# Performance work log

Measured on AMD Instinct MI355X. Metric: run time of the kernel, lower is better.

The kernel has to match this reference:

```python
import jax, jax.numpy as jnp
import numpy as np

V = 78864; E = 300; H = 512; A = 300; T = 20; DEC_EMB = 512; START = 2


def _pos_encoding(n, d):
    pos = np.arange(n)[:, None].astype(np.float32)
    i = np.arange(d)[None, :]
    angle = pos / np.power(10000.0, (2 * (i // 2)).astype(np.float32) / d)
    pe = np.where(i % 2 == 0, np.sin(angle), np.cos(angle)).astype(np.float32)
    return jnp.asarray(pe)  # [n, d]


def _lstm_cell(x, h, c, Wih, Whh, b):
    g = x @ Wih.T + h @ Whh.T + b
    i, f, gg, o = jnp.split(g, 4, axis=-1)
    c = jax.nn.sigmoid(f) * c + jax.nn.sigmoid(i) * jnp.tanh(gg)
    h = jax.nn.sigmoid(o) * jnp.tanh(c)
    return h, c


def setup_inputs() -> dict:
    key = jax.random.key(0)
    ks = iter(jax.random.split(key, 48))
    B, L = 40, 1000
    def w(shape, s=0.02):
        return jax.random.normal(next(ks), shape, jnp.float32) * s
    def z(shape):
        return jnp.zeros(shape, jnp.float32)
    inp = dict(
        enc_in=jax.random.randint(next(ks), (B, L), 0, V),
        enc_out=jax.random.normal(next(ks), (B, L, H), jnp.float32),
        enc_mask=jnp.zeros((B, L), bool),
        inputs=jax.random.randint(next(ks), (B, T), 0, V),
        embed=w((V, E)),
        elmo1_Wih=w((4 * H, E)), elmo1_Whh=w((4 * H, H)), elmo1_b=z((4 * H,)),
        elmo2_Wih=w((4 * H, H)), elmo2_Whh=w((4 * H, H)), elmo2_b=z((4 * H,)),
        in_W=w((DEC_EMB, H + E + A + H)), in_b=z((DEC_EMB,)),
        rnn1_Wih=w((4 * H, DEC_EMB)), rnn1_Whh=w((4 * H, H)), rnn1_b=z((4 * H,)),
        att1_Wq=w((A, H)), att1_bq=z((A,)), att1_Wk=w((A, H)), att1_bk=z((A,)), att1_Wv=w((A, H)), att1_bv=z((A,)),
        rnn2_Wih=w((4 * H, A)), rnn2_Whh=w((4 * H, H)), rnn2_b=z((4 * H,)),
        att2_Wq=w((A, H)), att2_bq=z((A,)), att2_Wk=w((A, H)), att2_bk=z((A,)), att2_Wv=w((A, H)), att2_bv=z((A,)),
        copy_W=w((A, H)), copy_b=z((A,)),
        out_W=w((V, A)), out_b=z((V,)),
        scale=jnp.asarray(1.0, jnp.float32),
    )
    return inp


def _forward(enc_in, enc_out, enc_mask, inputs, embed,
             elmo1_Wih, elmo1_Whh, elmo1_b, elmo2_Wih, elmo2_Whh, elmo2_b,
             in_W, in_b, rnn1_Wih, rnn1_Whh, rnn1_b,
             att1_Wq, att1_bq, att1_Wk, att1_bk, att1_Wv, att1_bv,
             rnn2_Wih, rnn2_Whh, rnn2_b,
             att2_Wq, att2_bq, att2_Wk, att2_bk, att2_Wv, att2_bv,
             copy_W, copy_b, out_W, out_b, scale):
    B, L = enc_in.shape
    pe = _pos_encoding(T, DEC_EMB)  # [T, 512]
    # Precompute per-encoder projections (hoisted out of the step loop).
    K1 = jnp.einsum('blh,ah->bla', enc_out, att1_Wk) + att1_bk
    V1 = jnp.einsum('blh,ah->bla', enc_out, att1_Wv) + att1_bv
    K2 = jnp.einsum('blh,ah->bla', enc_out, att2_Wk) + att2_bk
    V2 = jnp.einsum('blh,ah->bla', enc_out, att2_Wv) + att2_bv
    copyK = jnp.tanh(jnp.einsum('blh,ah->bla', enc_out, copy_W) + copy_b)
    bidx = jnp.arange(B)[:, None]

    def attn(h, Wq, bq, K, Vp):
        q = h @ Wq.T + bq                          # [B, A]
        s = jnp.einsum('ba,bla->bl', q, K)
        s = jnp.where(enc_mask, -1e9, s)
        p = jax.nn.softmax(s, axis=-1)
        return jnp.einsum('bl,bla->ba', p, Vp)

    # teacher forcing with random_int=0 -> always use ground-truth inputs
    sym_in = jnp.concatenate([jnp.full((B, 1), START, inputs.dtype), inputs[:, :-1]], axis=1).T  # [T,B]
    sym_out = inputs.T  # [T,B]

    zf = lambda *s: jnp.zeros(s, enc_out.dtype)
    carry0 = (zf(B, H), zf(B, H), zf(B, H), zf(B, H),  # elmo h1,c1,h2,c2
              zf(B, H), zf(B, H), zf(B, H), zf(B, H),  # rnn1 h,c ; rnn2 h,c
              zf(B, A), zf(B, H))                       # dec_att_out, select_read

    def step(carry, xs):
        eh1, ec1, eh2, ec2, h1, c1, h2, c2, att, sel = carry
        pe_t, s_in, s_out = xs
        emb = embed[s_in]                                           # [B, E]
        eh1, ec1 = _lstm_cell(emb, eh1, ec1, elmo1_Wih, elmo1_Whh, elmo1_b)
        eh2, ec2 = _lstm_cell(eh1, eh2, ec2, elmo2_Wih, elmo2_Whh, elmo2_b)
        in_embed = jnp.concatenate([emb, eh2], axis=-1)              # [B, 812]
        dec_in = jnp.concatenate([in_embed, att, sel], axis=-1) @ in_W.T + in_b + pe_t
        h1, c1 = _lstm_cell(dec_in, h1, c1, rnn1_Wih, rnn1_Whh, rnn1_b)
        att = attn(h1, att1_Wq, att1_bq, K1, V1)
        h2, c2 = _lstm_cell(att, h2, c2, rnn2_Wih, rnn2_Whh, rnn2_b)
        att = attn(h2, att2_Wq, att2_bq, K2, V2) + att
        # copy scores
        s = jnp.einsum('ba,bla->bl', att, copyK)
        s = jnp.where(enc_mask, -1e9, s)
        score_c = jax.nn.softmax(s, axis=-1)
        score_e = score_c * scale * scale
        vocab = att @ out_W.T + out_b                                # [B, V]
        vocab = vocab.at[bidx, enc_in].add(score_e)
        sym_pred = jnp.argmax(vocab, axis=-1).astype(jnp.int32)
        eq = (enc_in == s_out[:, None]).astype(score_c.dtype)
        score_f = score_c * eq
        score_f = score_f / (jnp.sum(score_f, axis=-1, keepdims=True) + 1e-8)
        sel = jnp.einsum('bl,blh->bh', score_f, enc_out)
        return (eh1, ec1, eh2, ec2, h1, c1, h2, c2, att, sel), (vocab, sym_pred)

    _, (dec_out, syms) = jax.lax.scan(step, carry0, (pe, sym_in, sym_out))
    return jnp.transpose(dec_out, (1, 0, 2)), syms.T  # [B,T,V], [B,T]


def reference(enc_in, enc_out, enc_mask, inputs, embed,
              elmo1_Wih, elmo1_Whh, elmo1_b, elmo2_Wih, elmo2_Whh, elmo2_b,
              in_W, in_b, rnn1_Wih, rnn1_Whh, rnn1_b,
              att1_Wq, att1_bq, att1_Wk, att1_bk, att1_Wv, att1_bv,
              rnn2_Wih, rnn2_Whh, rnn2_b,
              att2_Wq, att2_bq, att2_Wk, att2_bk, att2_Wv, att2_bv,
              copy_W, copy_b, out_W, out_b, scale):
    return _forward(enc_in, enc_out, enc_mask, inputs, embed,
                    elmo1_Wih, elmo1_Whh, elmo1_b, elmo2_Wih, elmo2_Whh, elmo2_b,
                    in_W, in_b, rnn1_Wih, rnn1_Whh, rnn1_b,
                    att1_Wq, att1_bq, att1_Wk, att1_bk, att1_Wv, att1_bv,
                    rnn2_Wih, rnn2_Whh, rnn2_b,
                    att2_Wq, att2_bq, att2_Wk, att2_bk, att2_Wv, att2_bv,
                    copy_W, copy_b, out_W, out_b, scale)
```

## Files before the change

### kernel.cpp

```cpp
#include <hip/hip_runtime.h>
#include <math.h>

#define B_ 40
#define L_ 1000
#define H_ 512
#define A_ 300
#define T_ 20
#define E_ 300
#define V_ 78864
#define START_ 2

#define NBLK 256
#define NTHR 512

#define OFF_COPYK 0ul
#define OFF_M1T   12000000ul
#define OFF_M2T   12262144ul
#define OFF_BQK1  12524288ul
#define OFF_BQK2  12524800ul
#define OFF_QK    12525312ul
#define OFF_DEC   12545792ul
#define OFF_ATT1  12566272ul
#define OFF_ATTT  12578272ul
#define OFF_CPART 12590272ul
#define OFF_CSTAT 12713152ul
#define OFF_SCC   12713664ul
#define OFF_STT   12753664ul
#define OFF_ATT2  13081344ul
#define OFF_SELP  13093344ul
#define OFF_CNT   13216224ul
#define WS_END    13216288ul

struct P {
  const int* enc_in; const float* enc; const unsigned char* mask; const int* inputs;
  const float* embed;
  const float *e1Wih,*e1Whh,*e1b,*e2Wih,*e2Whh,*e2b;
  const float *inW,*inb;
  const float *r1Wih,*r1Whh,*r1b;
  const float *a1Wq,*a1bq,*a1Wk,*a1Wv,*a1bv;
  const float *r2Wih,*r2Whh,*r2b;
  const float *a2Wq,*a2bq,*a2Wk,*a2Wv,*a2bv;
  const float *cW,*cb,*oW,*ob,*scale;
  float* dout;
  float *copyK,*M1T,*M2T,*bqk1,*bqk2,*qk,*dec,*att1,*attT,*cpart,*cstat,*scc,*stt,*att2,*selp;
  unsigned* cnt;
};

__device__ __forceinline__ float sigm(float x){ return 1.0f/(1.0f+expf(-x)); }

__device__ __forceinline__ float wredSum(float v){
#pragma unroll
  for(int o=32;o>0;o>>=1) v+=__shfl_xor(v,o);
  return v;
}
__device__ __forceinline__ float wredMax(float v){
#pragma unroll
  for(int o=32;o>0;o>>=1) v=fmaxf(v,__shfl_xor(v,o));
  return v;
}

__device__ __forceinline__ void gbar(unsigned* cnt, unsigned target){
  __syncthreads();
  if(threadIdx.x==0){
    __hip_atomic_fetch_add(cnt,1u,__ATOMIC_RELEASE,__HIP_MEMORY_SCOPE_AGENT);
    while(__hip_atomic_load(cnt,__ATOMIC_RELAXED,__HIP_MEMORY_SCOPE_AGENT)<target){
      __builtin_amdgcn_s_sleep(1);
    }
    (void)__hip_atomic_load(cnt,__ATOMIC_ACQUIRE,__HIP_MEMORY_SCOPE_AGENT);
  }
  __syncthreads();
}

template<typename SRC>
static __device__ __forceinline__ void gv_accum(float* xs,int K,const float* Wrow,
    float& acc,int lane,int kq,int nq,SRC src){
  for(int k0=0;k0<K;k0+=256){
    int ch=min(256,K-k0);
    __syncthreads();
    for(int i=threadIdx.x;i<40*ch;i+=NTHR){
      int bb=i/ch, kk=i-bb*ch;
      xs[bb*257+kk]=src(bb,k0+kk);
    }
    __syncthreads();
    if(lane<40){
#pragma unroll 4
      for(int k=kq;k<ch;k+=nq) acc+=Wrow[k0+k]*xs[lane*257+k];
    }
  }
}

static __device__ void lstm_ph(const P& p,float* SH,float* gld,int t,
    const float* Wih,int XD,const float* Whh,const float* bias,
    const float* xvec,bool gather,
    const float* hr,const float* cr,float* hw,float* cw){
  int tid=threadIdx.x,w=tid>>6,lane=tid&63;
  int gate=w&3,usub=w>>2;
  int row=gate*H_+(blockIdx.x*2+usub);
  int rowu=__builtin_amdgcn_readfirstlane(row);
  float acc=bias[rowu];
  const float* W1=Wih+(size_t)rowu*XD;
  if(gather){
    const int* inp=p.inputs; const float* emb=p.embed; int tt=t;
    gv_accum(SH,XD,W1,acc,lane,0,1,[=](int bb,int kk)->float{
      int si=(tt==0)?START_:inp[bb*T_+tt-1];
      return emb[(size_t)si*E_+kk];});
  }else{
    gv_accum(SH,XD,W1,acc,lane,0,1,[=](int bb,int kk)->float{
      return xvec[(size_t)bb*XD+kk];});
  }
  const float* W2=Whh+(size_t)rowu*H_;
  gv_accum(SH,H_,W2,acc,lane,0,1,[=](int bb,int kk)->float{
    return hr[bb*H_+kk];});
  gld[w*64+lane]=acc;
  __syncthreads();
  if(w<2&&lane<40){
    int u=blockIdx.x*2+w,b=lane;
    float gi=gld[(w*4+0)*64+b],gf=gld[(w*4+1)*64+b],gg=gld[(w*4+2)*64+b],go=gld[(w*4+3)*64+b];
    float c=cr[b*H_+u];
    float cn=sigm(gf)*c+sigm(gi)*tanhf(gg);
    hw[b*H_+u]=sigm(go)*tanhf(cn);
    cw[b*H_+u]=cn;
  }
  __syncthreads();
}

static __device__ void qk_ph(const P& p,float* SH,const float* hsrc,
    const float* MT,const float* bqk){
  int tid=threadIdx.x;
  if(blockIdx.x>=240) return;
  int b=blockIdx.x/6, j=blockIdx.x%6;
  SH[tid]=hsrc[b*H_+tid];
  __syncthreads();
  int h0=j*86, hc=min(86,H_-h0);
  if(tid<hc){
    int hp=h0+tid;
    float a=bqk[hp];
    const float4* mr=(const float4*)(MT+(size_t)hp*H_);
#pragma unroll 8
    for(int i=0;i<H_/4;i++){
      float4 m4=mr[i];
      a+=SH[4*i]*m4.x+SH[4*i+1]*m4.y+SH[4*i+2]*m4.z+SH[4*i+3]*m4.w;
    }
    p.qk[b*H_+hp]=a;
  }
}

static __device__ void scctx_ph(const P& p,float* SH,float* red){
  int tid=threadIdx.x,w=tid>>6,lane=tid&63;
  if(blockIdx.x>=240) return;
  int b=blockIdx.x/6, j=blockIdx.x%6;
  int l0=j*167, lcnt=min(167,L_-l0);
  const float* qrow=p.qk+b*H_;
  float4 q0=*(const float4*)(qrow+lane*8);
  float4 q1=*(const float4*)(qrow+lane*8+4);
  float m=-3.0e38f,S=0.f;
  float4 a0=make_float4(0.f,0.f,0.f,0.f), a1=a0;
  for(int l=l0+w;l<l0+lcnt;l+=8){
    const float4* er=(const float4*)(p.enc+((size_t)(b*L_+l))*H_);
    float4 e0=er[lane*2], e1=er[lane*2+1];
    float pp=q0.x*e0.x+q0.y*e0.y+q0.z*e0.z+q0.w*e0.w
            +q1.x*e1.x+q1.y*e1.y+q1.z*e1.z+q1.w*e1.w;
    pp=wredSum(pp);
    if(p.mask[b*L_+l]) pp=-1e9f;
    float mn=fmaxf(m,pp);
    float sc=expf(m-mn), pe=expf(pp-mn);
    S=S*sc+pe;
    a0.x=a0.x*sc+pe*e0.x; a0.y=a0.y*sc+pe*e0.y; a0.z=a0.z*sc+pe*e0.z; a0.w=a0.w*sc+pe*e0.w;
    a1.x=a1.x*sc+pe*e1.x; a1.y=a1.y*sc+pe*e1.y; a1.z=a1.z*sc+pe*e1.z; a1.w=a1.w*sc+pe*e1.w;
    m=mn;
  }
  *(float4*)(SH+w*H_+lane*8)=a0;
  *(float4*)(SH+w*H_+lane*8+4)=a1;
  if(lane==0){red[w]=m; red[8+w]=S;}
  __syncthreads();
  float mb=red[0];
#pragma unroll
  for(int q=1;q<8;q++) mb=fmaxf(mb,red[q]);
  float Sb=0.f;
#pragma unroll
  for(int q=0;q<8;q++) Sb+=red[8+q]*expf(red[q]-mb);
  float pv=0.f;
#pragma unroll
  for(int q=0;q<8;q++) pv+=expf(red[q]-mb)*SH[q*H_+tid];
  p.cpart[(size_t)(b*6+j)*H_+tid]=pv;
  if(tid==0){p.cstat[(b*6+j)*2]=mb; p.cstat[(b*6+j)*2+1]=Sb;}
}

static __device__ void atto_ph(const P& p,float* SH,const float* Wv,const float* bv,bool ADD){
  int tid=threadIdx.x;
  if(blockIdx.x>=40) return;
  int b=blockIdx.x;
  float mb=-3.0e38f;
#pragma unroll
  for(int j=0;j<6;j++) mb=fmaxf(mb,p.cstat[(b*6+j)*2]);
  float Sb=0.f;
#pragma unroll
  for(int j=0;j<6;j++) Sb+=p.cstat[(b*6+j)*2+1]*expf(p.cstat[(b*6+j)*2]-mb);
  float inv=1.0f/Sb;
  float cx=0.f;
#pragma unroll
  for(int j=0;j<6;j++) cx+=expf(p.cstat[(b*6+j)*2]-mb)*p.cpart[(size_t)(b*6+j)*H_+tid];
  SH[tid]=cx*inv;
  __syncthreads();
  if(tid<A_){
    float a=bv[tid];
    const float4* wr=(const float4*)(Wv+(size_t)tid*H_);
#pragma unroll 8
    for(int i=0;i<H_/4;i++){
      float4 w4=wr[i];
      a+=SH[4*i]*w4.x+SH[4*i+1]*w4.y+SH[4*i+2]*w4.z+SH[4*i+3]*w4.w;
    }
    if(ADD){ a+=p.att1[b*A_+tid]; p.att2[b*A_+tid]=a; p.attT[tid*B_+b]=a; }
    else p.att1[b*A_+tid]=a;
  }
}

static __device__ void copysc_ph(const P& p){
  int tid=threadIdx.x,w=tid>>6,lane=tid&63;
  if(blockIdx.x>=240) return;
  int b=blockIdx.x/6, j=blockIdx.x%6;
  int l0=j*167, lcnt=min(167,L_-l0);
  float4 r0=*(const float4*)(p.att2+b*A_+lane*4);
  float4 r1=make_float4(0.f,0.f,0.f,0.f);
  if(lane<11) r1=*(const float4*)(p.att2+b*A_+256+lane*4);
  for(int l=l0+w;l<l0+lcnt;l+=8){
    const float4* cr=(const float4*)(p.copyK+((size_t)(b*L_+l))*A_);
    float4 c0=cr[lane];
    float pp=r0.x*c0.x+r0.y*c0.y+r0.z*c0.z+r0.w*c0.w;
    if(lane<11){
      float4 c1=cr[64+lane];
      pp+=r1.x*c1.x+r1.y*c1.y+r1.z*c1.z+r1.w*c1.w;
    }
    pp=wredSum(pp);
    if(lane==0) p.scc[b*L_+l]=p.mask[b*L_+l]?-1e9f:pp;
  }
}

static __device__ void vocab_ph(const P& p,float* SH,int t){
  int tid=threadIdx.x;
  int v0=blockIdx.x*312;
  if(v0>=V_) return;
  int vcnt=min(312,V_-v0);
  float acc[40];
#pragma unroll
  for(int b=0;b<40;b++) acc[b]=0.f;
  for(int c=0;c<10;c++){
    int a0=c*32, aw=min(32,A_-a0);
    __syncthreads();
    for(int i=tid;i<vcnt*aw;i+=NTHR){
      int vr=i/aw, ac=i-vr*aw;
      SH[vr*33+ac]=p.oW[(size_t)(v0+vr)*A_+a0+ac];
    }
    __syncthreads();
    if(tid<vcnt){
      for(int ac=0;ac<aw;ac++){
        float wv=SH[tid*33+ac];
        const float* at=p.attT+(a0+ac)*B_;
#pragma unroll
        for(int bq=0;bq<10;bq++){
          float4 t4=*(const float4*)(at+bq*4);
          acc[bq*4+0]+=wv*t4.x; acc[bq*4+1]+=wv*t4.y;
          acc[bq*4+2]+=wv*t4.z; acc[bq*4+3]+=wv*t4.w;
        }
      }
    }
  }
  if(tid<vcnt){
    int v=v0+tid;
    float obv=p.ob[v];
#pragma unroll
    for(int b=0;b<40;b++) p.dout[((size_t)(b*T_+t))*V_+v]=acc[b]+obv;
  }
}

static __device__ void scatsel_ph(const P& p,float* SH,float* red,int t){
  int tid=threadIdx.x,w=tid>>6,lane=tid&63;
  if(blockIdx.x>=240) return;
  int b=blockIdx.x/6, j=blockIdx.x%6;
  int l0=j*167, lcnt=min(167,L_-l0);
  for(int i=tid;i<L_;i+=NTHR) SH[i]=p.scc[b*L_+i];
  __syncthreads();
  float lm=-3.0e38f;
  for(int i=tid;i<L_;i+=NTHR) lm=fmaxf(lm,SH[i]);
  lm=wredMax(lm);
  if(lane==0) red[w]=lm;
  __syncthreads();
  float m=red[0];
#pragma unroll
  for(int q=1;q<8;q++) m=fmaxf(m,red[q]);
  __syncthreads();
  int so=p.inputs[b*T_+t];
  float ls=0.f,lq=0.f;
  for(int i=tid;i<L_;i+=NTHR){
    float exv=expf(SH[i]-m);
    ls+=exv;
    if(p.enc_in[b*L_+i]==so) lq+=exv;
  }
  ls=wredSum(ls); lq=wredSum(lq);
  if(lane==0){red[w]=ls; red[8+w]=lq;}
  __syncthreads();
  float S=0.f,Q=0.f;
#pragma unroll
  for(int q=0;q<8;q++){S+=red[q];Q+=red[8+q];}
  if(tid<lcnt){
    int l=l0+tid;
    float exv=expf(SH[l]-m);
    SH[1024+tid]=(p.enc_in[b*L_+l]==so)?exv:0.f;
    float sc2=p.scale[0]*p.scale[0];
    atomicAdd(p.dout+((size_t)(b*T_+t))*V_+p.enc_in[b*L_+l], exv*sc2/S);
  }
  __syncthreads();
  float inv=1.0f/(Q+1e-8f*S);
  float a=0.f;
  for(int li=0;li<lcnt;li++)
    a+=SH[1024+li]*p.enc[((size_t)(b*L_+l0+li))*H_+tid];
  p.selp[(size_t)(b*6+j)*H_+tid]=a*inv;
}

static __device__ void argmax_ph(const P& p,float* SH,int t){
  int tid=threadIdx.x;
  if(blockIdx.x>=40) return;
  int b=blockIdx.x;
  const float* row=p.dout+((size_t)(b*T_+t))*V_;
  float best=-3.0e38f; int bi=0;
  for(int i4=tid;i4<V_/4;i4+=NTHR){
    float4 x=((const float4*)row)[i4];
    int base=i4*4;
    if(x.x>best){best=x.x;bi=base;}
    if(x.y>best){best=x.y;bi=base+1;}
    if(x.z>best){best=x.z;bi=base+2;}
    if(x.w>best){best=x.w;bi=base+3;}
  }
  int* isa=(int*)(SH+512);
  SH[tid]=best; isa[tid]=bi;
  __syncthreads();
  for(int off=256;off>0;off>>=1){
    if(tid<off){
      float ov=SH[tid+off]; int oi=isa[tid+off];
      if(ov>SH[tid]||(ov==SH[tid]&&oi<isa[tid])){SH[tid]=ov; isa[tid]=oi;}
    }
    __syncthreads();
  }
  if(tid==0) p.dout[(size_t)B_*T_*V_+b*T_+t]=(float)isa[0];
}

__global__ __launch_bounds__(NTHR,2) void k_persist(P p){
  __shared__ float SH[10320];
  __shared__ float gld[512];
  __shared__ float red[16];
  int blk=blockIdx.x, tid=threadIdx.x;
  unsigned bt=0;
#define BARR() do{bt++; gbar(p.cnt,bt*(unsigned)NBLK);}while(0)

  {
    int mm=blk>>7, r0=(blk&127)*4;
    const float* Wq = mm? p.a2Wq : p.a1Wq;
    const float* Wk = mm? p.a2Wk : p.a1Wk;
    float* MT = mm? p.M2T : p.M1T;
    float s0=0.f,s1=0.f,s2=0.f,s3=0.f;
    for(int a=0;a<A_;a++){
      float wq=Wq[a*H_+tid];
      s0+=wq*Wk[a*H_+r0+0];
      s1+=wq*Wk[a*H_+r0+1];
      s2+=wq*Wk[a*H_+r0+2];
      s3+=wq*Wk[a*H_+r0+3];
    }
    MT[(size_t)(r0+0)*H_+tid]=s0;
    MT[(size_t)(r0+1)*H_+tid]=s1;
    MT[(size_t)(r0+2)*H_+tid]=s2;
    MT[(size_t)(r0+3)*H_+tid]=s3;
    if((blk&127)==0){
      const float* bq = mm? p.a2bq : p.a1bq;
      float ab=0.f;
      for(int a=0;a<A_;a++) ab+=bq[a]*Wk[a*H_+tid];
      (mm? p.bqk2 : p.bqk1)[tid]=ab;
    }
  }
  for(int item=blk;item<B_*63;item+=NBLK){
    int b=item/63, lt=item-b*63;
    int l0=lt*16, lcnt=min(16,L_-l0);
    float acc[16];
    float bv=(tid<A_)?p.cb[tid]:0.f;
#pragma unroll
    for(int l=0;l<16;l++) acc[l]=bv;
    for(int k0=0;k0<H_;k0+=32){
      __syncthreads();
      for(int i=tid;i<A_*32;i+=NTHR){
        int a=i>>5,kc=i&31;
        SH[a*33+kc]=p.cW[(size_t)a*H_+k0+kc];
      }
      __syncthreads();
      if(tid<A_){
#pragma unroll
        for(int l=0;l<16;l++){
          if(l<lcnt){
            const float* es=p.enc+((size_t)(b*L_+l0+l))*H_+k0;
            float al=acc[l];
#pragma unroll
            for(int kc=0;kc<32;kc++) al+=SH[tid*33+kc]*es[kc];
            acc[l]=al;
          }
        }
      }
    }
    if(tid<A_){
#pragma unroll
      for(int l=0;l<16;l++)
        if(l<lcnt) p.copyK[((size_t)(b*L_+l0+l))*A_+tid]=tanhf(acc[l]);
    }
  }
  BARR();

  for(int t=0;t<T_;t++){
    int rp=t&1, wp=rp^1;
    float* stt=p.stt;
    auto SL=[&](int i,int par){ return stt+((size_t)(i*2+par))*(B_*H_); };
    float *eh1r=SL(0,rp),*eh1w=SL(0,wp),*ec1r=SL(1,rp),*ec1w=SL(1,wp);
    float *eh2r=SL(2,rp),*eh2w=SL(2,wp),*ec2r=SL(3,rp),*ec2w=SL(3,wp);
    float *h1r=SL(4,rp),*h1w=SL(4,wp),*c1r=SL(5,rp),*c1w=SL(5,wp);
    float *h2r=SL(6,rp),*h2w=SL(6,wp),*c2r=SL(7,rp),*c2w=SL(7,wp);

    lstm_ph(p,SH,gld,t,p.e1Wih,E_,p.e1Whh,p.e1b,nullptr,true ,eh1r,ec1r,eh1w,ec1w); BARR();
    lstm_ph(p,SH,gld,t,p.e2Wih,H_,p.e2Whh,p.e2b,eh1w  ,false,eh2r,ec2r,eh2w,ec2w); BARR();

    {
      int w=tid>>6,lane=tid&63;
      int usub=w>>2, kq=w&3;
      int unit=blk*2+usub;
      int rowu=__builtin_amdgcn_readfirstlane(unit);
      float acc=0.f;
      const float* Wr=p.inW+(size_t)rowu*1624;
      const int* inp=p.inputs; const float* emb=p.embed;
      const float* e2=eh2w; const float* a2c=p.att2; const float* sp=p.selp;
      int tt=t;
      gv_accum(SH,1624,Wr,acc,lane,kq,4,[=](int bb,int kk)->float{
        if(kk<E_){int si=(tt==0)?START_:inp[bb*T_+tt-1];return emb[(size_t)si*E_+kk];}
        else if(kk<E_+H_) return e2[bb*H_+kk-E_];
        else if(kk<E_+H_+A_) return a2c[bb*A_+kk-(E_+H_)];
        else{
          int hh=kk-(E_+H_+A_); float s=0.f;
#pragma unroll
          for(int jj=0;jj<6;jj++) s+=sp[(size_t)(bb*6+jj)*H_+hh];
          return s;
        }
      });
      gld[(usub*4+kq)*64+lane]=acc;
      __syncthreads();
      if(w<2&&lane<40){
        int u=blk*2+w;
        float s=gld[(w*4+0)*64+lane]+gld[(w*4+1)*64+lane]
               +gld[(w*4+2)*64+lane]+gld[(w*4+3)*64+lane];
        float ex=(float)(2*(u>>1))/512.0f;
        float ang=(float)t/powf(10000.0f,ex);
        s+=p.inb[u]+((u&1)?cosf(ang):sinf(ang));
        p.dec[lane*H_+u]=s;
      }
      __syncthreads();
    }
    BARR();

    lstm_ph(p,SH,gld,t,p.r1Wih,H_,p.r1Whh,p.r1b,p.dec ,false,h1r,c1r,h1w,c1w); BARR();
    qk_ph(p,SH,h1w,p.M1T,p.bqk1);                                              BARR();
    scctx_ph(p,SH,red);                                                        BARR();
    atto_ph(p,SH,p.a1Wv,p.a1bv,false);                                         BARR();
    lstm_ph(p,SH,gld,t,p.r2Wih,A_,p.r2Whh,p.r2b,p.att1,false,h2r,c2r,h2w,c2w); BARR();
    qk_ph(p,SH,h2w,p.M2T,p.bqk2);                                              BARR();
    scctx_ph(p,SH,red);                                                        BARR();
    atto_ph(p,SH,p.a2Wv,p.a2bv,true);                                          BARR();
    copysc_ph(p);                                                              BARR();
    vocab_ph(p,SH,t);                                                          BARR();
    scatsel_ph(p,SH,red,t);                                                    BARR();
    argmax_ph(p,SH,t);
  }
#undef BARR
}

extern "C" void kernel_launch(void* const* d_in, const int* in_sizes, int n_in,
                              void* d_out, int out_size, void* d_ws, size_t ws_size,
                              hipStream_t stream){
  P p;
  p.enc_in=(const int*)d_in[0];
  p.enc   =(const float*)d_in[1];
  p.mask  =(const unsigned char*)d_in[2];
  p.inputs=(const int*)d_in[3];
  p.embed =(const float*)d_in[4];
  p.e1Wih=(const float*)d_in[5];  p.e1Whh=(const float*)d_in[6];  p.e1b=(const float*)d_in[7];
  p.e2Wih=(const float*)d_in[8];  p.e2Whh=(const float*)d_in[9];  p.e2b=(const float*)d_in[10];
  p.inW  =(const float*)d_in[11]; p.inb  =(const float*)d_in[12];
  p.r1Wih=(const float*)d_in[13]; p.r1Whh=(const float*)d_in[14]; p.r1b=(const float*)d_in[15];
  p.a1Wq =(const float*)d_in[16]; p.a1bq =(const float*)d_in[17];
  p.a1Wk =(const float*)d_in[18];
  p.a1Wv =(const float*)d_in[20]; p.a1bv =(const float*)d_in[21];
  p.r2Wih=(const float*)d_in[22]; p.r2Whh=(const float*)d_in[23]; p.r2b=(const float*)d_in[24];
  p.a2Wq =(const float*)d_in[25]; p.a2bq =(const float*)d_in[26];
  p.a2Wk =(const float*)d_in[27];
  p.a2Wv =(const float*)d_in[29]; p.a2bv =(const float*)d_in[30];
  p.cW   =(const float*)d_in[31]; p.cb   =(const float*)d_in[32];
  p.oW   =(const float*)d_in[33]; p.ob   =(const float*)d_in[34];
  p.scale=(const float*)d_in[35];
  p.dout=(float*)d_out;

  float* w=(float*)d_ws;
  p.copyK=w+OFF_COPYK;
  p.M1T  =w+OFF_M1T;   p.M2T =w+OFF_M2T;
  p.bqk1 =w+OFF_BQK1;  p.bqk2=w+OFF_BQK2;
  p.qk   =w+OFF_QK;    p.dec =w+OFF_DEC;
  p.att1 =w+OFF_ATT1;  p.attT=w+OFF_ATTT;
  p.cpart=w+OFF_CPART; p.cstat=w+OFF_CSTAT;
  p.scc  =w+OFF_SCC;   p.stt =w+OFF_STT;
  p.att2 =w+OFF_ATT2;  p.selp=w+OFF_SELP;
  p.cnt  =(unsigned*)(w+OFF_CNT);

  hipMemsetAsync(w+OFF_STT,0,(WS_END-OFF_STT)*sizeof(float),stream);
  k_persist<<<NBLK,NTHR,0,stream>>>(p);
}
```

Before: 18.03 ms.

## Store copy keys as padded bf16 and restructure attention context via LDS tiles

```diff
diff --git a/kernel.cpp b/kernel.cpp
--- a/kernel.cpp
+++ b/kernel.cpp
@@ -13,23 +13,23 @@
 #define NBLK 256
 #define NTHR 512
 
-#define OFF_COPYK 0ul
-#define OFF_M1T   12000000ul
-#define OFF_M2T   12262144ul
-#define OFF_BQK1  12524288ul
-#define OFF_BQK2  12524800ul
-#define OFF_QK    12525312ul
-#define OFF_DEC   12545792ul
-#define OFF_ATT1  12566272ul
-#define OFF_ATTT  12578272ul
-#define OFF_CPART 12590272ul
-#define OFF_CSTAT 12713152ul
-#define OFF_SCC   12713664ul
-#define OFF_STT   12753664ul
-#define OFF_ATT2  13081344ul
-#define OFF_SELP  13093344ul
-#define OFF_CNT   13216224ul
-#define WS_END    13216288ul
+#define OFF_CKH   0ul
+#define OFF_M1T   6400000ul
+#define OFF_M2T   6662144ul
+#define OFF_BQK1  6924288ul
+#define OFF_BQK2  6924800ul
+#define OFF_QK    6925312ul
+#define OFF_DEC   6945792ul
+#define OFF_ATT1  6966272ul
+#define OFF_ATTT  6978272ul
+#define OFF_CPART 6990272ul
+#define OFF_CSTAT 7113152ul
+#define OFF_SCC   7113664ul
+#define OFF_STT   7153664ul
+#define OFF_ATT2  7481344ul
+#define OFF_SELP  7493344ul
+#define OFF_CNT   7616224ul
+#define WS_END    7616288ul
 
 struct P {
   const int* enc_in; const float* enc; const unsigned char* mask; const int* inputs;
@@ -42,7 +42,8 @@
   const float *a2Wq,*a2bq,*a2Wk,*a2Wv,*a2bv;
   const float *cW,*cb,*oW,*ob,*scale;
   float* dout;
-  float *copyK,*M1T,*M2T,*bqk1,*bqk2,*qk,*dec,*att1,*attT,*cpart,*cstat,*scc,*stt,*att2,*selp;
+  unsigned short* copyKh;
+  float *M1T,*M2T,*bqk1,*bqk2,*qk,*dec,*att1,*attT,*cpart,*cstat,*scc,*stt,*att2,*selp;
   unsigned* cnt;
 };
 
@@ -57,6 +58,11 @@
 #pragma unroll
   for(int o=32;o>0;o>>=1) v=fmaxf(v,__shfl_xor(v,o));
   return v;
+}
+__device__ __forceinline__ unsigned short f2bf(float f){
+  unsigned u=__float_as_uint(f);
+  u=(u+0x7fffu+((u>>16)&1u))>>16;
+  return (unsigned short)u;
 }
 
 __device__ __forceinline__ void gbar(unsigned* cnt, unsigned target){
@@ -145,7 +151,7 @@
   }
 }
 
-static __device__ void scctx_ph(const P& p,float* SH,float* red){
+static __device__ void scctx_ph(const P& p,float* SH){
   int tid=threadIdx.x,w=tid>>6,lane=tid&63;
   if(blockIdx.x>=240) return;
   int b=blockIdx.x/6, j=blockIdx.x%6;
@@ -153,37 +159,49 @@
   const float* qrow=p.qk+b*H_;
   float4 q0=*(const float4*)(qrow+lane*8);
   float4 q1=*(const float4*)(qrow+lane*8+4);
-  float m=-3.0e38f,S=0.f;
-  float4 a0=make_float4(0.f,0.f,0.f,0.f), a1=a0;
-  for(int l=l0+w;l<l0+lcnt;l+=8){
-    const float4* er=(const float4*)(p.enc+((size_t)(b*L_+l))*H_);
-    float4 e0=er[lane*2], e1=er[lane*2+1];
-    float pp=q0.x*e0.x+q0.y*e0.y+q0.z*e0.z+q0.w*e0.w
-            +q1.x*e1.x+q1.y*e1.y+q1.z*e1.z+q1.w*e1.w;
-    pp=wredSum(pp);
-    if(p.mask[b*L_+l]) pp=-1e9f;
-    float mn=fmaxf(m,pp);
-    float sc=expf(m-mn), pe=expf(pp-mn);
-    S=S*sc+pe;
-    a0.x=a0.x*sc+pe*e0.x; a0.y=a0.y*sc+pe*e0.y; a0.z=a0.z*sc+pe*e0.z; a0.w=a0.w*sc+pe*e0.w;
-    a1.x=a1.x*sc+pe*e1.x; a1.y=a1.y*sc+pe*e1.y; a1.z=a1.z*sc+pe*e1.z; a1.w=a1.w*sc+pe*e1.w;
+  float* tile=SH;
+  float* sc16=SH+8192;
+  float m=-3.0e38f,S=0.f,acc=0.f;
+  for(int t0=0;t0<lcnt;t0+=16){
+    int tc=min(16,lcnt-t0);
+    __syncthreads();
+    {
+      const float4* src=(const float4*)(p.enc+((size_t)(b*L_+l0+t0))*H_);
+      float4* dst=(float4*)tile;
+      for(int i=tid;i<tc*128;i+=NTHR) dst[i]=src[i];
+    }
+    __syncthreads();
+#pragma unroll
+    for(int r=0;r<2;r++){
+      int row=w*2+r;
+      float sc;
+      if(row<tc){
+        const float4* er=(const float4*)(tile+row*512);
+        float4 e0=er[lane*2], e1=er[lane*2+1];
+        float pp=q0.x*e0.x+q0.y*e0.y+q0.z*e0.z+q0.w*e0.w
+                +q1.x*e1.x+q1.y*e1.y+q1.z*e1.z+q1.w*e1.w;
+        pp=wredSum(pp);
+        sc=p.mask[b*L_+l0+t0+row]?-1e9f:pp;
+      } else sc=-1e30f;
+      if(lane==0) sc16[row]=sc;
+    }
+    __syncthreads();
+    float tm=-3.0e38f;
+    for(int r=0;r<tc;r++) tm=fmaxf(tm,sc16[r]);
+    float mn=fmaxf(m,tm);
+    float scl=expf(m-mn);
+    float Sadd=0.f, aadd=0.f;
+    for(int r=0;r<tc;r++){
+      float pe=expf(sc16[r]-mn);
+      Sadd+=pe;
+      aadd+=pe*tile[r*512+tid];
+    }
+    S=S*scl+Sadd;
+    acc=acc*scl+aadd;
     m=mn;
   }
-  *(float4*)(SH+w*H_+lane*8)=a0;
-  *(float4*)(SH+w*H_+lane*8+4)=a1;
-  if(lane==0){red[w]=m; red[8+w]=S;}
-  __syncthreads();
-  float mb=red[0];
-#pragma unroll
-  for(int q=1;q<8;q++) mb=fmaxf(mb,red[q]);
-  float Sb=0.f;
-#pragma unroll
-  for(int q=0;q<8;q++) Sb+=red[8+q]*expf(red[q]-mb);
-  float pv=0.f;
-#pragma unroll
-  for(int q=0;q<8;q++) pv+=expf(red[q]-mb)*SH[q*H_+tid];
-  p.cpart[(size_t)(b*6+j)*H_+tid]=pv;
-  if(tid==0){p.cstat[(b*6+j)*2]=mb; p.cstat[(b*6+j)*2+1]=Sb;}
+  p.cpart[(size_t)(b*6+j)*H_+tid]=acc;
+  if(tid==0){p.cstat[(b*6+j)*2]=m; p.cstat[(b*6+j)*2+1]=S;}
 }
 
 static __device__ void atto_ph(const P& p,float* SH,const float* Wv,const float* bv,bool ADD){
@@ -220,16 +238,21 @@
   if(blockIdx.x>=240) return;
   int b=blockIdx.x/6, j=blockIdx.x%6;
   int l0=j*167, lcnt=min(167,L_-l0);
-  float4 r0=*(const float4*)(p.att2+b*A_+lane*4);
-  float4 r1=make_float4(0.f,0.f,0.f,0.f);
-  if(lane<11) r1=*(const float4*)(p.att2+b*A_+256+lane*4);
+  float ar[8];
+#pragma unroll
+  for(int q=0;q<8;q++){
+    int a=lane*8+q;
+    ar[q]=(lane<40&&a<A_)? p.att2[b*A_+a] : 0.f;
+  }
   for(int l=l0+w;l<l0+lcnt;l+=8){
-    const float4* cr=(const float4*)(p.copyK+((size_t)(b*L_+l))*A_);
-    float4 c0=cr[lane];
-    float pp=r0.x*c0.x+r0.y*c0.y+r0.z*c0.z+r0.w*c0.w;
-    if(lane<11){
-      float4 c1=cr[64+lane];
-      pp+=r1.x*c1.x+r1.y*c1.y+r1.z*c1.z+r1.w*c1.w;
+    float pp=0.f;
+    if(lane<40){
+      const uint4* cr=(const uint4*)(p.copyKh+((size_t)(b*L_+l))*320);
+      uint4 kk=cr[lane];
+      pp =ar[0]*__uint_as_float(kk.x<<16)+ar[1]*__uint_as_float(kk.x&0xffff0000u);
+      pp+=ar[2]*__uint_as_float(kk.y<<16)+ar[3]*__uint_as_float(kk.y&0xffff0000u);
+      pp+=ar[4]*__uint_as_float(kk.z<<16)+ar[5]*__uint_as_float(kk.z&0xffff0000u);
+      pp+=ar[6]*__uint_as_float(kk.w<<16)+ar[7]*__uint_as_float(kk.w&0xffff0000u);
     }
     pp=wredSum(pp);
     if(lane==0) p.scc[b*L_+l]=p.mask[b*L_+l]?-1e9f:pp;
@@ -246,10 +269,13 @@
   for(int b=0;b<40;b++) acc[b]=0.f;
   for(int c=0;c<10;c++){
     int a0=c*32, aw=min(32,A_-a0);
-    __syncthreads();
-    for(int i=tid;i<vcnt*aw;i+=NTHR){
-      int vr=i/aw, ac=i-vr*aw;
-      SH[vr*33+ac]=p.oW[(size_t)(v0+vr)*A_+a0+ac];
+    int awf4=aw>>2;
+    __syncthreads();
+    for(int i=tid;i<vcnt*awf4;i+=NTHR){
+      int vr=i/awf4, f=i-vr*awf4;
+      float4 x=*(const float4*)(p.oW+(size_t)(v0+vr)*A_+a0+f*4);
+      float* dst=&SH[vr*33+f*4];
+      dst[0]=x.x;dst[1]=x.y;dst[2]=x.z;dst[3]=x.w;
     }
     __syncthreads();
     if(tid<vcnt){
@@ -403,10 +429,15 @@
         }
       }
     }
-    if(tid<A_){
-#pragma unroll
-      for(int l=0;l<16;l++)
-        if(l<lcnt) p.copyK[((size_t)(b*L_+l0+l))*A_+tid]=tanhf(acc[l]);
+    if(tid<320){
+#pragma unroll
+      for(int l=0;l<16;l++){
+        if(l<lcnt){
+          unsigned short hv=0;
+          if(tid<A_) hv=f2bf(tanhf(acc[l]));
+          p.copyKh[((size_t)(b*L_+l0+l))*320+tid]=hv;
+        }
+      }
     }
   }
   BARR();
@@ -461,11 +492,11 @@
 
     lstm_ph(p,SH,gld,t,p.r1Wih,H_,p.r1Whh,p.r1b,p.dec ,false,h1r,c1r,h1w,c1w); BARR();
     qk_ph(p,SH,h1w,p.M1T,p.bqk1);                                              BARR();
-    scctx_ph(p,SH,red);                                                        BARR();
+    scctx_ph(p,SH);                                                            BARR();
     atto_ph(p,SH,p.a1Wv,p.a1bv,false);                                         BARR();
     lstm_ph(p,SH,gld,t,p.r2Wih,A_,p.r2Whh,p.r2b,p.att1,false,h2r,c2r,h2w,c2w); BARR();
     qk_ph(p,SH,h2w,p.M2T,p.bqk2);                                              BARR();
-    scctx_ph(p,SH,red);                                                        BARR();
+    scctx_ph(p,SH);                                                            BARR();
     atto_ph(p,SH,p.a2Wv,p.a2bv,true);                                          BARR();
     copysc_ph(p);                                                              BARR();
     vocab_ph(p,SH,t);                                                          BARR();
@@ -501,7 +532,7 @@
   p.dout=(float*)d_out;
 
   float* w=(float*)d_ws;
-  p.copyK=w+OFF_COPYK;
+  p.copyKh=(unsigned short*)(w+OFF_CKH);
   p.M1T  =w+OFF_M1T;   p.M2T =w+OFF_M2T;
   p.bqk1 =w+OFF_BQK1;  p.bqk2=w+OFF_BQK2;
   p.qk   =w+OFF_QK;    p.dec =w+OFF_DEC;
```

Measured after the change: 18.66 ms. 1.03x slower.
